# Optimization experiments

Hardware: AMD Instinct MI355X
Metric: run time of the kernel (lower is better)

Reference implementation:

```python
import jax, jax.numpy as jnp
import numpy as np

B, D, H = 4096, 1024, 1024
LN_EPS = 1e-5


def setup_inputs() -> dict:
    key = jax.random.key(0)
    ks = jax.random.split(key, 5)
    return {
        "x": jax.random.normal(ks[0], (B, D), dtype=jnp.float32),
        "prev_h": jax.random.normal(ks[1], (B, H), dtype=jnp.float32),
        "prev_c": jax.random.normal(ks[2], (B, H), dtype=jnp.float32),
        "Wx": jax.random.normal(ks[3], (D, 4 * H), dtype=jnp.float32) * 0.01,
        "Wh": jax.random.normal(ks[4], (H, 4 * H), dtype=jnp.float32) * 0.01,
        "b": jnp.zeros((4 * H,), dtype=jnp.float32),
        "ln_gamma": jnp.ones((4 * H,), dtype=jnp.float32),
        "ln_beta": jnp.zeros((4 * H,), dtype=jnp.float32),
    }


def reference(x, prev_h, prev_c, Wx, Wh, b, ln_gamma, ln_beta):
    # pre-activations: [B, 4H]
    a = x @ Wx + prev_h @ Wh + b
    # LayerNorm over last dim (use_ln=True)
    mu = jnp.mean(a, axis=-1, keepdims=True)
    var = jnp.mean(jnp.square(a - mu), axis=-1, keepdims=True)
    a = (a - mu) * jax.lax.rsqrt(var + LN_EPS) * ln_gamma + ln_beta
    i = jax.nn.sigmoid(a[:, :H])
    f = jax.nn.sigmoid(a[:, H:2 * H])
    o = jax.nn.sigmoid(a[:, 2 * H:3 * H])
    g = jnp.tanh(a[:, 3 * H:])
    next_c = f * prev_c + i * g
    next_h = o * jnp.tanh(next_c)
    # dropout=0.0 -> identity
    return (next_h, next_c)
```

## Files before the change

### kernel.cpp

```cpp
#include <hip/hip_runtime.h>
#include <hip/hip_bf16.h>
#include <stdint.h>

typedef unsigned short u16;
typedef __attribute__((ext_vector_type(8))) short short8;
typedef __attribute__((ext_vector_type(16))) float f32x16;

#define B_DIM 4096
#define D_DIM 1024
#define H_DIM 1024
#define K_DIM 2048
#define N_DIM 4096
#define LN_EPS 1e-5f

__device__ __forceinline__ u16 f2bf(float f) {
    union { float f; uint32_t u; } v; v.f = f;
    uint32_t u = v.u;
    uint32_t r = (u + 0x7FFFu + ((u >> 16) & 1u)) >> 16;
    return (u16)r;
}
__device__ __forceinline__ float bf2f(u16 h) {
    union { uint32_t u; float f; } v; v.u = ((uint32_t)h) << 16;
    return v.f;
}
__device__ __forceinline__ void gld16(const u16* g, u16* l) {
    __builtin_amdgcn_global_load_lds(
        (const __attribute__((address_space(1))) void*)g,
        (__attribute__((address_space(3))) void*)l,
        16, 0, 0);
}
__device__ __forceinline__ float sigm(float x) { return 1.0f / (1.0f + __expf(-x)); }
__device__ __forceinline__ float tanh_fast(float x) { return 1.0f - 2.0f / (__expf(2.0f * x) + 1.0f); }

__global__ __launch_bounds__(256) void prep(const float* __restrict__ x,
                                            const float* __restrict__ h,
                                            const float* __restrict__ Wx,
                                            const float* __restrict__ Wh,
                                            u16* __restrict__ A,
                                            u16* __restrict__ Bt) {
    __shared__ u16 tile[64 * 64];
    const int t = threadIdx.x;
    if (blockIdx.x < 4096) {
        int id = blockIdx.x * 256 + t;
        int row = id >> 8;
        int col = (id & 255) * 8;
        const float* src = (col < D_DIM) ? (x + (size_t)row * D_DIM + col)
                                         : (h + (size_t)row * H_DIM + (col - D_DIM));
        float4 v0 = ((const float4*)src)[0];
        float4 v1 = ((const float4*)src)[1];
        union { u16 us[8]; uint4 u; } p;
        p.us[0] = f2bf(v0.x); p.us[1] = f2bf(v0.y); p.us[2] = f2bf(v0.z); p.us[3] = f2bf(v0.w);
        p.us[4] = f2bf(v1.x); p.us[5] = f2bf(v1.y); p.us[6] = f2bf(v1.z); p.us[7] = f2bf(v1.w);
        *(uint4*)(A + (size_t)id * 8) = p.u;
    } else {
        const int v = blockIdx.x - 4096;
        const int n0 = (v & 63) * 64;
        const int k0 = (v >> 6) * 64;
        const int kl  = t >> 4;
        const int nl4 = (t & 15) * 4;
#pragma unroll
        for (int it = 0; it < 4; ++it) {
            const int klocal = kl + it * 16;
            const int k = k0 + klocal;
            const float* src = (k < D_DIM) ? (Wx + (size_t)k * N_DIM)
                                           : (Wh + (size_t)(k - D_DIM) * N_DIM);
            float4 w = *(const float4*)(src + n0 + nl4);
            union { u16 us[4]; uint2 u; } p;
            p.us[0] = f2bf(w.x); p.us[1] = f2bf(w.y); p.us[2] = f2bf(w.z); p.us[3] = f2bf(w.w);
            const int swz = 8 * ((klocal >> 4) & 3);
            *(uint2*)(tile + klocal * 64 + (nl4 ^ swz)) = p.u;
        }
        __syncthreads();
        const int nl = t >> 2;
        const int kp = (t & 3) * 16;
        const int swz = 8 * (t & 3);
        union { u16 us[16]; uint4 q[2]; } o;
#pragma unroll
        for (int i = 0; i < 16; ++i)
            o.us[i] = tile[(kp + i) * 64 + (nl ^ swz)];
        u16* dst = Bt + (size_t)(n0 + nl) * K_DIM + k0 + kp;
        *(uint4*)dst = o.q[0];
        *(uint4*)(dst + 8) = o.q[1];
    }
}

__global__ __launch_bounds__(256) void gemm_bf16(const u16* __restrict__ A,
                                                 const u16* __restrict__ Bt,
                                                 const float* __restrict__ bias,
                                                 u16* __restrict__ C) {
    __shared__ u16 As[128 * 64];
    __shared__ u16 Bs[128 * 64];
    const int m0 = blockIdx.y * 128;
    const int n0 = blockIdx.x * 128;
    const int tid = threadIdx.x;
    const int wave = tid >> 6, lane = tid & 63;
    const int wm = (wave & 1) * 64, wn = (wave >> 1) * 64;

    f32x16 acc[2][2] = {};

    const int kbg = ((lane & 7) - ((lane >> 3) & 7)) & 7;
    const int skc = kbg * 8;
    const u16* aG = A  + (size_t)(m0 + wave * 32 + (lane >> 3)) * K_DIM + skc;
    const u16* bG = Bt + (size_t)(n0 + wave * 32 + (lane >> 3)) * K_DIM + skc;
    u16* aL = As + (wave * 32) * 64;
    u16* bL = Bs + (wave * 32) * 64;

    const int lr = lane & 31;
    const int half = lane >> 5;
    const u16* aFbase = As + (size_t)(wm + lr) * 64;
    const u16* bFbase = Bs + (size_t)(wn + lr) * 64;

    for (int kt = 0; kt < K_DIM; kt += 64) {
        __syncthreads();
#pragma unroll
        for (int q = 0; q < 4; ++q) {
            gld16(aG + kt + (size_t)q * 8 * K_DIM, aL + q * 8 * 64);
            gld16(bG + kt + (size_t)q * 8 * K_DIM, bL + q * 8 * 64);
        }
        __syncthreads();

#pragma unroll
        for (int kk = 0; kk < 4; ++kk) {
            const int koff = (((kk * 2 + half) + (lr & 7)) & 7) * 8;
            short8 af[2], bf[2];
#pragma unroll
            for (int i = 0; i < 2; ++i)
                af[i] = *(const short8*)(aFbase + i * 32 * 64 + koff);
#pragma unroll
            for (int j = 0; j < 2; ++j)
                bf[j] = *(const short8*)(bFbase + j * 32 * 64 + koff);
#pragma unroll
            for (int i = 0; i < 2; ++i)
#pragma unroll
                for (int j = 0; j < 2; ++j)
                    acc[i][j] = __builtin_amdgcn_mfma_f32_32x32x16_bf16(af[i], bf[j], acc[i][j], 0, 0, 0);
        }
    }

#pragma unroll
    for (int i = 0; i < 2; ++i) {
#pragma unroll
        for (int j = 0; j < 2; ++j) {
            const int c = n0 + wn + 32 * j + lr;
            const float bb = bias[c];
#pragma unroll
            for (int reg = 0; reg < 16; ++reg) {
                const int row = m0 + wm + 32 * i + (reg & 3) + 8 * (reg >> 2) + 4 * half;
                C[(size_t)row * N_DIM + c] = f2bf(acc[i][j][reg] + bb);
            }
        }
    }
}

__global__ __launch_bounds__(256) void ln_lstm(const u16* __restrict__ aT,
                                               const float* __restrict__ pc,
                                               const float* __restrict__ gamma,
                                               const float* __restrict__ beta,
                                               float* __restrict__ out) {
    const int row = blockIdx.x;
    const int t = threadIdx.x;
    const u16* ar = aT + (size_t)row * N_DIM;
    const int j0 = t * 4;

    union U2 { uint2 u; u16 us[4]; };
    U2 g4[4];
#pragma unroll
    for (int s = 0; s < 4; ++s) g4[s].u = *(const uint2*)(ar + s * H_DIM + j0);

    float sum = 0.f, ssq = 0.f;
#pragma unroll
    for (int s = 0; s < 4; ++s)
#pragma unroll
        for (int e = 0; e < 4; ++e) { float v = bf2f(g4[s].us[e]); sum += v; ssq += v * v; }

#pragma unroll
    for (int off = 32; off > 0; off >>= 1) {
        sum += __shfl_down(sum, off, 64);
        ssq += __shfl_down(ssq, off, 64);
    }
    __shared__ float red[8];
    if ((t & 63) == 0) { red[t >> 6] = sum; red[4 + (t >> 6)] = ssq; }
    __syncthreads();
    const float ts = red[0] + red[1] + red[2] + red[3];
    const float tq = red[4] + red[5] + red[6] + red[7];
    const float mu = ts * (1.0f / N_DIM);
    const float var = fmaxf(tq * (1.0f / N_DIM) - mu * mu, 0.0f);
    const float rs = rsqrtf(var + LN_EPS);

    float vi[4], vf[4], vo[4], vg[4];
    auto gate = [&](int s, float* v) {
        const int off = s * H_DIM;
        float4 gm = *(const float4*)(gamma + off + j0);
        float4 bt = *(const float4*)(beta + off + j0);
        v[0] = (bf2f(g4[s].us[0]) - mu) * rs * gm.x + bt.x;
        v[1] = (bf2f(g4[s].us[1]) - mu) * rs * gm.y + bt.y;
        v[2] = (bf2f(g4[s].us[2]) - mu) * rs * gm.z + bt.z;
        v[3] = (bf2f(g4[s].us[3]) - mu) * rs * gm.w + bt.w;
    };
    gate(0, vi); gate(1, vf); gate(2, vo); gate(3, vg);

    float4 c4 = *(const float4*)(pc + (size_t)row * H_DIM + j0);
    float cin[4] = {c4.x, c4.y, c4.z, c4.w};
    float nh[4], nc[4];
#pragma unroll
    for (int r = 0; r < 4; ++r) {
        float ig = sigm(vi[r]);
        float fg = sigm(vf[r]);
        float og = sigm(vo[r]);
        float gg = tanh_fast(vg[r]);
        nc[r] = fg * cin[r] + ig * gg;
        nh[r] = og * tanh_fast(nc[r]);
    }
    float4 h4 = {nh[0], nh[1], nh[2], nh[3]};
    float4 c4o = {nc[0], nc[1], nc[2], nc[3]};
    *(float4*)(out + (size_t)row * H_DIM + j0) = h4;
    *(float4*)(out + (size_t)B_DIM * H_DIM + (size_t)row * H_DIM + j0) = c4o;
}

extern "C" void kernel_launch(void* const* d_in, const int* in_sizes, int n_in,
                              void* d_out, int out_size, void* d_ws, size_t ws_size,
                              hipStream_t stream) {
    const float* x  = (const float*)d_in[0];
    const float* ph = (const float*)d_in[1];
    const float* pc = (const float*)d_in[2];
    const float* Wx = (const float*)d_in[3];
    const float* Wh = (const float*)d_in[4];
    const float* b  = (const float*)d_in[5];
    const float* gm = (const float*)d_in[6];
    const float* bt = (const float*)d_in[7];
    float* out = (float*)d_out;

    char* ws = (char*)d_ws;
    u16* Abf = (u16*)ws;
    u16* Btb = (u16*)(ws + (size_t)16 * 1024 * 1024);
    u16* aT  = (u16*)(ws + (size_t)32 * 1024 * 1024);

    prep<<<dim3(4096 + 2048), dim3(256), 0, stream>>>(x, ph, Wx, Wh, Abf, Btb);
    gemm_bf16<<<dim3(32, 32), dim3(256), 0, stream>>>(Abf, Btb, b, aT);
    ln_lstm<<<dim3(4096), dim3(256), 0, stream>>>(aT, pc, gm, bt, out);
}
```

Measured before the change: 229.5 us.

## Enlarge GEMM tile to 256x256 with double-buffered LDS prefetch

The bf16 GEMM block tile grows from 128x128 to 256x256, so each wave now computes a 128x128 sub-tile using a 4x4 set of MFMA accumulators. LDS is double-buffered so the global-to-LDS load for the next K step is issued before the MFMAs on the current buffer, leaving one barrier per iteration. This aims to raise data reuse per byte loaded and to hide load latency behind compute. The cost is 128 KB of LDS and a large register footprint, giving one block per CU. The grid also shrinks to 256 blocks, which may leave CUs idle on a 256-CU part.

```diff
diff --git a/kernel.cpp b/kernel.cpp
--- a/kernel.cpp
+++ b/kernel.cpp
@@ -84,63 +84,67 @@
     }
 }
 
-__global__ __launch_bounds__(256) void gemm_bf16(const u16* __restrict__ A,
-                                                 const u16* __restrict__ Bt,
-                                                 const float* __restrict__ bias,
-                                                 u16* __restrict__ C) {
-    __shared__ u16 As[128 * 64];
-    __shared__ u16 Bs[128 * 64];
-    const int m0 = blockIdx.y * 128;
-    const int n0 = blockIdx.x * 128;
+__global__ __launch_bounds__(256, 1) void gemm_bf16(const u16* __restrict__ A,
+                                                    const u16* __restrict__ Bt,
+                                                    const float* __restrict__ bias,
+                                                    u16* __restrict__ C) {
+    __shared__ u16 As[2][256 * 64];
+    __shared__ u16 Bs[2][256 * 64];
     const int tid = threadIdx.x;
     const int wave = tid >> 6, lane = tid & 63;
-    const int wm = (wave & 1) * 64, wn = (wave >> 1) * 64;
-
-    f32x16 acc[2][2] = {};
-
-    const int kbg = ((lane & 7) - ((lane >> 3) & 7)) & 7;
-    const int skc = kbg * 8;
-    const u16* aG = A  + (size_t)(m0 + wave * 32 + (lane >> 3)) * K_DIM + skc;
-    const u16* bG = Bt + (size_t)(n0 + wave * 32 + (lane >> 3)) * K_DIM + skc;
-    u16* aL = As + (wave * 32) * 64;
-    u16* bL = Bs + (wave * 32) * 64;
-
-    const int lr = lane & 31;
-    const int half = lane >> 5;
-    const u16* aFbase = As + (size_t)(wm + lr) * 64;
-    const u16* bFbase = Bs + (size_t)(wn + lr) * 64;
-
-    for (int kt = 0; kt < K_DIM; kt += 64) {
+    const int m0 = blockIdx.y * 256;
+    const int n0 = blockIdx.x * 256;
+    const int wm = (wave & 1) * 128;
+    const int wn = (wave >> 1) * 128;
+
+    f32x16 acc[4][4] = {};
+
+    const int skc = (((lane & 7) - (lane >> 3) - 2 * wave + 32) & 7) * 8;
+    const u16* aG = A  + (size_t)(m0 + wave * 8 + (lane >> 3)) * K_DIM + skc;
+    const u16* bG = Bt + (size_t)(n0 + wave * 8 + (lane >> 3)) * K_DIM + skc;
+    const int ldsOff = (wave * 8) * 64;
+
+    const int lr = lane & 31, half = lane >> 5;
+    const int permR = ((lr & 7) + 2 * (lr >> 3)) & 7;
+
+    for (int it = 0; it < K_DIM / 64 + 1; ++it) {
+        if (it < K_DIM / 64) {
+            const int kt = it * 64;
+            const int buf = it & 1;
+            u16* aL = &As[buf][ldsOff];
+            u16* bL = &Bs[buf][ldsOff];
+#pragma unroll
+            for (int q = 0; q < 8; ++q) {
+                gld16(aG + kt + (size_t)q * 32 * K_DIM, aL + q * 32 * 64);
+                gld16(bG + kt + (size_t)q * 32 * K_DIM, bL + q * 32 * 64);
+            }
+        }
+        if (it == 0) { __syncthreads(); continue; }
+
+        const int cbuf = (it - 1) & 1;
+#pragma unroll
+        for (int kk = 0; kk < 4; ++kk) {
+            const int koff = (((kk * 2 + half) + permR) & 7) * 8;
+            short8 af[4], bf[4];
+#pragma unroll
+            for (int i = 0; i < 4; ++i)
+                af[i] = *(const short8*)(&As[cbuf][(wm + i * 32 + lr) * 64 + koff]);
+#pragma unroll
+            for (int j = 0; j < 4; ++j)
+                bf[j] = *(const short8*)(&Bs[cbuf][(wn + j * 32 + lr) * 64 + koff]);
+#pragma unroll
+            for (int i = 0; i < 4; ++i)
+#pragma unroll
+                for (int j = 0; j < 4; ++j)
+                    acc[i][j] = __builtin_amdgcn_mfma_f32_32x32x16_bf16(af[i], bf[j], acc[i][j], 0, 0, 0);
+        }
         __syncthreads();
-#pragma unroll
-        for (int q = 0; q < 4; ++q) {
-            gld16(aG + kt + (size_t)q * 8 * K_DIM, aL + q * 8 * 64);
-            gld16(bG + kt + (size_t)q * 8 * K_DIM, bL + q * 8 * 64);
-        }
-        __syncthreads();
-
-#pragma unroll
-        for (int kk = 0; kk < 4; ++kk) {
-            const int koff = (((kk * 2 + half) + (lr & 7)) & 7) * 8;
-            short8 af[2], bf[2];
-#pragma unroll
-            for (int i = 0; i < 2; ++i)
-                af[i] = *(const short8*)(aFbase + i * 32 * 64 + koff);
-#pragma unroll
-            for (int j = 0; j < 2; ++j)
-                bf[j] = *(const short8*)(bFbase + j * 32 * 64 + koff);
-#pragma unroll
-            for (int i = 0; i < 2; ++i)
-#pragma unroll
-                for (int j = 0; j < 2; ++j)
-                    acc[i][j] = __builtin_amdgcn_mfma_f32_32x32x16_bf16(af[i], bf[j], acc[i][j], 0, 0, 0);
-        }
-    }
-
-#pragma unroll
-    for (int i = 0; i < 2; ++i) {
-#pragma unroll
-        for (int j = 0; j < 2; ++j) {
+    }
+
+#pragma unroll
+    for (int i = 0; i < 4; ++i) {
+#pragma unroll
+        for (int j = 0; j < 4; ++j) {
             const int c = n0 + wn + 32 * j + lr;
             const float bb = bias[c];
 #pragma unroll
@@ -236,6 +240,6 @@
     u16* aT  = (u16*)(ws + (size_t)32 * 1024 * 1024);
 
     prep<<<dim3(4096 + 2048), dim3(256), 0, stream>>>(x, ph, Wx, Wh, Abf, Btb);
-    gemm_bf16<<<dim3(32, 32), dim3(256), 0, stream>>>(Abf, Btb, b, aT);
+    gemm_bf16<<<dim3(16, 16), dim3(256), 0, stream>>>(Abf, Btb, b, aT);
     ln_lstm<<<dim3(4096), dim3(256), 0, stream>>>(aT, pc, gm, bt, out);
 }
```

New measurement: 228.4 us. Within noise of the previous version (-0.5%).
